# Kernel tuning notes

Measured on AMD Instinct MI355X. Metric: run time of the kernel, lower is better.

Reference implementation:

```python
import jax, jax.numpy as jnp
import numpy as np

N_PIXELS = 262144
N_CENTERS = 1024
N_G = 256

def setup_inputs() -> dict:
    key = jax.random.key(0)
    k1, k2, k3, k4, k5 = jax.random.split(key, 5)
    return {
        "alphas": jax.random.normal(k1, (N_CENTERS, 1), dtype=jnp.float32),
        "betas": jax.random.normal(k2, (N_G, 2), dtype=jnp.float32) * 0.1,
        "K": jax.random.normal(k3, (N_PIXELS, N_G), dtype=jnp.float32) * 0.05,
        "all_pixels": jax.random.normal(k4, (N_PIXELS, 2), dtype=jnp.float32),
        "all_p_centers": jax.random.normal(k5, (N_CENTERS, 2), dtype=jnp.float32),
        "sdp2": jnp.ones((), dtype=jnp.float32) * 2.0,
    }

def reference(alphas, betas, K, all_pixels, all_p_centers, sdp2):
    # deformed pixel coordinates: (n_pixels, 2)
    deformed = all_pixels - K @ betas
    # pairwise squared distances via norm expansion (same math as the torch
    # ones-matmul broadcasting, expressed with plain broadcasting):
    p_norm2 = jnp.sum(jnp.square(deformed), axis=1, keepdims=True)      # (n_pixels, 1)
    c_norm2 = jnp.sum(jnp.square(all_p_centers), axis=1)                # (n_centers,)
    p_dot_c = 2.0 * (deformed @ all_p_centers.T)                        # (n_pixels, n_centers)
    big_matrix = p_norm2 + c_norm2[None, :] - p_dot_c
    kBp = jnp.exp(-big_matrix / (2.0 * sdp2))
    return kBp @ alphas                                                  # (n_pixels, 1)
```

## Files before the change

### kernel.cpp

```cpp
#include <hip/hip_runtime.h>

#if defined(__has_builtin)
#  if __has_builtin(__builtin_amdgcn_exp2f)
#    define EXP2F(x) __builtin_amdgcn_exp2f(x)
#  else
#    define EXP2F(x) exp2f(x)
#  endif
#else
#  define EXP2F(x) exp2f(x)
#endif

constexpr int NPIX  = 262144;
constexpr int NC    = 1024;
constexpr int NG    = 256;
constexpr int BLOCK = 256;
constexpr int GRID  = NPIX / 512;

template <int CTRL>
__device__ __forceinline__ float dpp_add(float v) {
    union { float f; int i; } u, t;
    u.f = v;
    t.i = __builtin_amdgcn_update_dpp(0, u.i, CTRL, 0xF, 0xF, true);
    return v + t.f;
}
template <int CTRL>
__device__ __forceinline__ float dpp_mov(float v) {
    union { float f; int i; } u, t;
    u.f = v;
    t.i = __builtin_amdgcn_update_dpp(0, u.i, CTRL, 0xF, 0xF, true);
    return t.f;
}
__device__ __forceinline__ float sum64_lane63(float v) {
    v = dpp_add<0xB1>(v);
    v = dpp_add<0x4E>(v);
    v = dpp_add<0x141>(v);
    v = dpp_add<0x140>(v);
    v = dpp_add<0x142>(v);
    v = dpp_add<0x143>(v);
    return v;
}
__device__ __forceinline__ float readlane63(float v) {
    union { float f; int i; } u; u.f = v;
    union { int i; float f; } r;
    r.i = __builtin_amdgcn_readlane(u.i, 63);
    return r.f;
}

#define LOAD4(BUF, ABSROW)                                                   \
    _Pragma("unroll")                                                        \
    for (int j = 0; j < 4; ++j)                                              \
        BUF[j] = ((const float4*)(K + (size_t)((ABSROW) + j) * NG))[lane];

#define RED4(BUF, REL, PX, DXO, DYO)                                         \
    _Pragma("unroll")                                                        \
    for (int j = 0; j < 4; ++j) {                                            \
        float sx = BUF[j].x * bb0.x + BUF[j].y * bb0.z;                      \
        float sy = BUF[j].x * bb0.y + BUF[j].y * bb0.w;                      \
        sx = fmaf(BUF[j].z, bb1.x, sx); sy = fmaf(BUF[j].z, bb1.y, sy);      \
        sx = fmaf(BUF[j].w, bb1.z, sx); sy = fmaf(BUF[j].w, bb1.w, sy);      \
        sx = sum64_lane63(sx); sy = sum64_lane63(sy);                        \
        const float tx = readlane63(sx);                                     \
        const float ty = readlane63(sy);                                     \
        if (lane == (REL) + j) { DXO = PX.x - tx; DYO = PX.y - ty; }         \
    }

#define BSTEPS(N)                                                            \
    _Pragma("unroll")                                                        \
    for (int t = 0; t < (N); ++t) {                                          \
        float t0 = 0.f, t1 = 0.f, t2 = 0.f, t3 = 0.f;                        \
        _Pragma("unroll")                                                    \
        for (int j = 0; j < 4; ++j) {                                        \
            t0 = fmaf(rca[j].x, EXP2F(fmaf(dxs, rcx[j].x, dys * rcy[j].x)), t0); \
            t1 = fmaf(rca[j].y, EXP2F(fmaf(dxs, rcx[j].y, dys * rcy[j].y)), t1); \
            t2 = fmaf(rca[j].z, EXP2F(fmaf(dxs, rcx[j].z, dys * rcy[j].z)), t2); \
            t3 = fmaf(rca[j].w, EXP2F(fmaf(dxs, rcx[j].w, dys * rcy[j].w)), t3); \
        }                                                                    \
        acc += (t0 + t1) + (t2 + t3);                                        \
        dxs = dpp_mov<0x121>(dxs);                            \
        dys = dpp_mov<0x121>(dys);                                           \
        acc = dpp_mov<0x121>(acc);                                           \
    }

__global__ __launch_bounds__(BLOCK, 2)
void kbpa_pipe(const float* __restrict__ alphas,
               const float* __restrict__ betas,
               const float* __restrict__ K,
               const float* __restrict__ pixels,
               const float* __restrict__ centers,
               const float* __restrict__ sdp2p,
               float* __restrict__ out)
{
    const int lane = threadIdx.x & 63;
    const int wave = threadIdx.x >> 6;

    const int cpx = GRID / 8;
    const int bid = (blockIdx.x & 7) * cpx + (blockIdx.x >> 3);

    const float f   = -1.44269504088896340736f / (2.0f * sdp2p[0]);
    const float m2f = -2.0f * f;

    float4 rcx[4], rcy[4], rca[4];
    {
        const float4* c4 = (const float4*)centers;
        const float4* a4 = (const float4*)alphas;
        #pragma unroll
        for (int j = 0; j < 4; ++j) {
            const float4 p0 = c4[lane * 8 + 2 * j];
            const float4 p1 = c4[lane * 8 + 2 * j + 1];
            rcx[j] = make_float4(p0.x, p0.z, p1.x, p1.z);
            rcy[j] = make_float4(p0.y, p0.w, p1.y, p1.w);
            const float4 al = a4[lane * 4 + j];
            rca[j].x = al.x * EXP2F(f * (rcx[j].x * rcx[j].x + rcy[j].x * rcy[j].x));
            rca[j].y = al.y * EXP2F(f * (rcx[j].y * rcx[j].y + rcy[j].y * rcy[j].y));
            rca[j].z = al.z * EXP2F(f * (rcx[j].z * rcx[j].z + rcy[j].z * rcy[j].z));
            rca[j].w = al.w * EXP2F(f * (rcx[j].w * rcx[j].w + rcy[j].w * rcy[j].w));
        }
    }

    const float4* bf4 = (const float4*)betas;
    const float4 bb0 = bf4[2 * lane];
    const float4 bb1 = bf4[2 * lane + 1];

    const int w0 = bid * 512 + wave * 128;
    const int w1 = w0 + 64;
    const float2 px0 = ((const float2*)pixels)[w0 + lane];
    const float2 px1 = ((const float2*)pixels)[w1 + lane];

    float dx0 = 0.f, dy0 = 0.f, dx1 = 0.f, dy1 = 0.f;
    float4 kva[4], kvb[4];

    LOAD4(kva, w0 + 0)
    #pragma unroll 1
    for (int gg = 0; gg < 8; ++gg) {
        const int g = 2 * gg;
        LOAD4(kvb, w0 + (g + 1) * 4)
        RED4(kva, g * 4, px0, dx0, dy0)
        if (gg < 7) { LOAD4(kva, w0 + (g + 2) * 4) }
        RED4(kvb, (g + 1) * 4, px0, dx0, dy0)
    }

    float dxs = m2f * dx0, dys = m2f * dy0, acc = 0.f;
    LOAD4(kva, w1 + 0)
    #pragma unroll 1
    for (int gg = 0; gg < 8; ++gg) {
        const int g = 2 * gg;
        LOAD4(kvb, w1 + (g + 1) * 4)
        BSTEPS(4)
        RED4(kva, g * 4, px1, dx1, dy1)
        if (gg < 7) { LOAD4(kva, w1 + (g + 2) * 4) }
        BSTEPS(4)
        RED4(kvb, (g + 1) * 4, px1, dx1, dy1)
        if (gg & 1) {
            const int sw = lane ^ ((gg & 2) ? 32 : 16);
            dxs = __shfl(dxs, sw);
            dys = __shfl(dys, sw);
            acc = __shfl(acc, sw);
        }
    }
    out[w0 + lane] = acc * EXP2F(f * (dx0 * dx0 + dy0 * dy0));

    dxs = m2f * dx1; dys = m2f * dy1; acc = 0.f;
    #pragma unroll 1
    for (int round = 0; round < 4; ++round) {
        BSTEPS(16)
        const int sw = lane ^ ((round & 1) ? 32 : 16);
        dxs = __shfl(dxs, sw);
        dys = __shfl(dys, sw);
        acc = __shfl(acc, sw);
    }
    out[w1 + lane] = acc * EXP2F(f * (dx1 * dx1 + dy1 * dy1));
}

extern "C" void kernel_launch(void* const* d_in, const int* in_sizes, int n_in,
                              void* d_out, int out_size, void* d_ws, size_t ws_size,
                              hipStream_t stream)
{
    const float* alphas  = (const float*)d_in[0];
    const float* betas   = (const float*)d_in[1];
    const float* K       = (const float*)d_in[2];
    const float* pixels  = (const float*)d_in[3];
    const float* centers = (const float*)d_in[4];
    const float* sdp2    = (const float*)d_in[5];
    float* outp          = (float*)d_out;

    hipLaunchKernelGGL(kbpa_pipe, dim3(GRID), dim3(BLOCK), 0, stream,
                       alphas, betas, K, pixels, centers, sdp2, outp);
}
```

Baseline: 72.44 us.

## Split block into producer waves for K@betas and consumer waves for exp-sum

Blocks grow to 512 threads. Four producer waves stream K rows and reduce the deformation offsets into shared memory, publishing each 64-pixel group with a flag. Four consumer waves spin on those flags and run the exp/accumulate loop over all 1024 centers. This replaces the hand-interleaved software pipeline inside each wave with warp specialization, so memory-bound and compute-bound work overlap across waves. The risks are load imbalance: producers idle once their eight groups are done, consumers wait at startup, and only half the waves do the exp-heavy work.

```diff
diff --git a/kernel.cpp b/kernel.cpp
--- a/kernel.cpp
+++ b/kernel.cpp
@@ -10,11 +10,12 @@
 #  define EXP2F(x) exp2f(x)
 #endif
 
-constexpr int NPIX  = 262144;
-constexpr int NC    = 1024;
-constexpr int NG    = 256;
-constexpr int BLOCK = 256;
-constexpr int GRID  = NPIX / 512;
+constexpr int NPIX    = 262144;
+constexpr int NC      = 1024;
+constexpr int NG      = 256;
+constexpr int THREADS = 512;
+constexpr int PPB     = 512;
+constexpr int GRID    = NPIX / PPB;
 
 template <int CTRL>
 __device__ __forceinline__ float dpp_add(float v) {
@@ -51,7 +52,7 @@
     for (int j = 0; j < 4; ++j)                                              \
         BUF[j] = ((const float4*)(K + (size_t)((ABSROW) + j) * NG))[lane];
 
-#define RED4(BUF, REL, PX, DXO, DYO)                                         \
+#define RED4(BUF, REL)                                                       \
     _Pragma("unroll")                                                        \
     for (int j = 0; j < 4; ++j) {                                            \
         float sx = BUF[j].x * bb0.x + BUF[j].y * bb0.z;                      \
@@ -61,7 +62,7 @@
         sx = sum64_lane63(sx); sy = sum64_lane63(sy);                        \
         const float tx = readlane63(sx);                                     \
         const float ty = readlane63(sy);                                     \
-        if (lane == (REL) + j) { DXO = PX.x - tx; DYO = PX.y - ty; }         \
+        if (lane == (REL) + j) { osx = tx; osy = ty; }                       \
     }
 
 #define BSTEPS(N)                                                            \
@@ -81,94 +82,100 @@
         acc = dpp_mov<0x121>(acc);                                           \
     }
 
-__global__ __launch_bounds__(BLOCK, 2)
-void kbpa_pipe(const float* __restrict__ alphas,
-               const float* __restrict__ betas,
-               const float* __restrict__ K,
-               const float* __restrict__ pixels,
-               const float* __restrict__ centers,
-               const float* __restrict__ sdp2p,
-               float* __restrict__ out)
+__global__ __launch_bounds__(THREADS, 2)
+void kbpa_pc(const float* __restrict__ alphas,
+             const float* __restrict__ betas,
+             const float* __restrict__ K,
+             const float* __restrict__ pixels,
+             const float* __restrict__ centers,
+             const float* __restrict__ sdp2p,
+             float* __restrict__ out)
 {
-    const int lane = threadIdx.x & 63;
-    const int wave = threadIdx.x >> 6;
+    __shared__ float2 sxy_sh[PPB];
+    __shared__ int    flags[8];
 
-    const int cpx = GRID / 8;
-    const int bid = (blockIdx.x & 7) * cpx + (blockIdx.x >> 3);
+    const int tid  = threadIdx.x;
+    const int lane = tid & 63;
+    const int wv   = tid >> 6;
 
-    const float f   = -1.44269504088896340736f / (2.0f * sdp2p[0]);
-    const float m2f = -2.0f * f;
+    const int bid  = (blockIdx.x & 7) * (GRID / 8) + (blockIdx.x >> 3);
+    const int base = bid * PPB;
 
-    float4 rcx[4], rcy[4], rca[4];
-    {
-        const float4* c4 = (const float4*)centers;
-        const float4* a4 = (const float4*)alphas;
-        #pragma unroll
-        for (int j = 0; j < 4; ++j) {
-            const float4 p0 = c4[lane * 8 + 2 * j];
-            const float4 p1 = c4[lane * 8 + 2 * j + 1];
-            rcx[j] = make_float4(p0.x, p0.z, p1.x, p1.z);
-            rcy[j] = make_float4(p0.y, p0.w, p1.y, p1.w);
-            const float4 al = a4[lane * 4 + j];
-            rca[j].x = al.x * EXP2F(f * (rcx[j].x * rcx[j].x + rcy[j].x * rcy[j].x));
-            rca[j].y = al.y * EXP2F(f * (rcx[j].y * rcx[j].y + rcy[j].y * rcy[j].y));
-            rca[j].z = al.z * EXP2F(f * (rcx[j].z * rcx[j].z + rcy[j].z * rcy[j].z));
-            rca[j].w = al.w * EXP2F(f * (rcx[j].w * rcx[j].w + rcy[j].w * rcy[j].w));
+    if (tid < 8) flags[tid] = 0;
+    __syncthreads();
+
+    const float f = -1.44269504088896340736f / (2.0f * sdp2p[0]);
+
+    if (wv < 4) {
+        const float4* bf4 = (const float4*)betas;
+        const float4 bb0 = bf4[2 * lane];
+        const float4 bb1 = bf4[2 * lane + 1];
+
+        #pragma unroll 1
+        for (int chunk = 0; chunk < 2; ++chunk) {
+            const int grp = wv * 2 + chunk;
+            const int r0  = base + grp * 64;
+            float osx = 0.f, osy = 0.f;
+            float4 kva[4], kvb[4];
+
+            LOAD4(kva, r0)
+            #pragma unroll 1
+            for (int gg = 0; gg < 8; ++gg) {
+                const int g = 2 * gg;
+                LOAD4(kvb, r0 + (g + 1) * 4)
+                RED4(kva, g * 4)
+                if (gg < 7) { LOAD4(kva, r0 + (g + 2) * 4) }
+                RED4(kvb, (g + 1) * 4)
+            }
+            sxy_sh[grp * 64 + lane] = make_float2(osx, osy);
+            __threadfence_block();
+            if (lane == 0) ((volatile int*)flags)[grp] = 1;
+        }
+    } else {
+        const float m2f = -2.0f * f;
+        float4 rcx[4], rcy[4], rca[4];
+        {
+            const float4* c4 = (const float4*)centers;
+            const float4* a4 = (const float4*)alphas;
+            #pragma unroll
+            for (int j = 0; j < 4; ++j) {
+                const float4 p0 = c4[lane * 8 + 2 * j];
+                const float4 p1 = c4[lane * 8 + 2 * j + 1];
+                rcx[j] = make_float4(p0.x, p0.z, p1.x, p1.z);
+                rcy[j] = make_float4(p0.y, p0.w, p1.y, p1.w);
+                const float4 al = a4[lane * 4 + j];
+                rca[j].x = al.x * EXP2F(f * (rcx[j].x * rcx[j].x + rcy[j].x * rcy[j].x));
+                rca[j].y = al.y * EXP2F(f * (rcx[j].y * rcx[j].y + rcy[j].y * rcy[j].y));
+                rca[j].z = al.z * EXP2F(f * (rcx[j].z * rcx[j].z + rcy[j].z * rcy[j].z));
+                rca[j].w = al.w * EXP2F(f * (rcx[j].w * rcx[j].w + rcy[j].w * rcy[j].w));
+            }
+        }
+
+        const int b = wv - 4;
+        #pragma unroll 1
+        for (int grp = 2 * b; grp < 2 * b + 2; ++grp) {
+            while (((volatile int*)flags)[grp] == 0)
+                __builtin_amdgcn_s_sleep(2);
+            __threadfence_block();
+
+            const int p = base + grp * 64 + lane;
+            const float2 s  = sxy_sh[grp * 64 + lane];
+            const float2 px = ((const float2*)pixels)[p];
+            const float dx = px.x - s.x;
+            const float dy = px.y - s.y;
+
+            float dxs = m2f * dx, dys = m2f * dy, acc = 0.f;
+            #pragma unroll 1
+            for (int round = 0; round < 4; ++round) {
+                BSTEPS(16)
+                const int sw = lane ^ ((round & 1) ? 32 : 16);
+                dxs = __shfl(dxs, sw);
+                dys = __shfl(dys, sw);
+                acc = __shfl(acc, sw);
+            }
+            out[p] = acc * EXP2F(f * (dx * dx + dy * dy));
         }
     }
-
-    const float4* bf4 = (const float4*)betas;
-    const float4 bb0 = bf4[2 * lane];
-    const float4 bb1 = bf4[2 * lane + 1];
-
-    const int w0 = bid * 512 + wave * 128;
-    const int w1 = w0 + 64;
-    const float2 px0 = ((const float2*)pixels)[w0 + lane];
-    const float2 px1 = ((const float2*)pixels)[w1 + lane];
-
-    float dx0 = 0.f, dy0 = 0.f, dx1 = 0.f, dy1 = 0.f;
-    float4 kva[4], kvb[4];
-
-    LOAD4(kva, w0 + 0)
-    #pragma unroll 1
-    for (int gg = 0; gg < 8; ++gg) {
-        const int g = 2 * gg;
-        LOAD4(kvb, w0 + (g + 1) * 4)
-        RED4(kva, g * 4, px0, dx0, dy0)
-        if (gg < 7) { LOAD4(kva, w0 + (g + 2) * 4) }
-        RED4(kvb, (g + 1) * 4, px0, dx0, dy0)
-    }
-
-    float dxs = m2f * dx0, dys = m2f * dy0, acc = 0.f;
-    LOAD4(kva, w1 + 0)
-    #pragma unroll 1
-    for (int gg = 0; gg < 8; ++gg) {
-        const int g = 2 * gg;
-        LOAD4(kvb, w1 + (g + 1) * 4)
-        BSTEPS(4)
-        RED4(kva, g * 4, px1, dx1, dy1)
-        if (gg < 7) { LOAD4(kva, w1 + (g + 2) * 4) }
-        BSTEPS(4)
-        RED4(kvb, (g + 1) * 4, px1, dx1, dy1)
-        if (gg & 1) {
-            const int sw = lane ^ ((gg & 2) ? 32 : 16);
-            dxs = __shfl(dxs, sw);
-            dys = __shfl(dys, sw);
-            acc = __shfl(acc, sw);
-        }
-    }
-    out[w0 + lane] = acc * EXP2F(f * (dx0 * dx0 + dy0 * dy0));
-
-    dxs = m2f * dx1; dys = m2f * dy1; acc = 0.f;
-    #pragma unroll 1
-    for (int round = 0; round < 4; ++round) {
-        BSTEPS(16)
-        const int sw = lane ^ ((round & 1) ? 32 : 16);
-        dxs = __shfl(dxs, sw);
-        dys = __shfl(dys, sw);
-        acc = __shfl(acc, sw);
-    }
-    out[w1 + lane] = acc * EXP2F(f * (dx1 * dx1 + dy1 * dy1));
 }
 
 extern "C" void kernel_launch(void* const* d_in, const int* in_sizes, int n_in,
@@ -183,6 +190,6 @@
     const float* sdp2    = (const float*)d_in[5];
     float* outp          = (float*)d_out;
 
-    hipLaunchKernelGGL(kbpa_pipe, dim3(GRID), dim3(BLOCK), 0, stream,
+    hipLaunchKernelGGL(kbpa_pc, dim3(GRID), dim3(THREADS), 0, stream,
                        alphas, betas, K, pixels, centers, sdp2, outp);
 }
```

After: 73.99 us. +2.1%, slower.
